# Optimization experiments

Hardware: AMD Instinct MI355X
Metric: run time of the kernel (lower is better)

The kernel has to match this reference:

```python
import jax, jax.numpy as jnp
import numpy as np

APERTURE = 256
IGNORE_ITSELF = False
FMAX = jnp.float32(3.4028235e38)  # tf.float32.max


def setup_inputs() -> dict:
    key = jax.random.key(0)
    ks = jax.random.split(key, 5)
    n, m, d = 4096, 1024, 1024
    scale = 1.0 / np.sqrt(m)
    x = jax.random.normal(ks[0], (n, m), dtype=jnp.float32)
    WK = jax.random.normal(ks[1], (m, d), dtype=jnp.float32) * scale
    WQ = jax.random.normal(ks[2], (m, d), dtype=jnp.float32) * scale
    WV = jax.random.normal(ks[3], (m, d), dtype=jnp.float32) * scale
    Wout = jax.random.normal(ks[4], (d, m), dtype=jnp.float32) * scale
    return {"x": x, "WK": WK, "WQ": WQ, "WV": WV, "Wout": Wout}


def reference(x, WK, WQ, WV, Wout):
    n = x.shape[0]
    K = x @ WK                      # [n, d]
    Q = (x @ WQ) * 0.06             # [n, d]
    V = x @ WV                      # [n, d]
    logits = Q @ K.T                # [n, n]

    i = jnp.arange(n)[:, None]
    j = jnp.arange(n)[None, :]
    if IGNORE_ITSELF:
        keep = (i != j).astype(jnp.float32)
        logits = logits * keep - FMAX * (1.0 - keep)
    if APERTURE > 0:
        # tf: mask = 1 - band_part(ones, -aperture, aperture); negative num_lower
        # keeps the whole lower triangle, so mask==1 exactly where j - i > aperture.
        keep = (j - i > APERTURE).astype(jnp.float32)
        logits = logits * keep - FMAX * (1.0 - keep)

    att_weights = jax.nn.softmax(logits, axis=-1)  # [n, n]
    # dropout is identity (training=False). NOTE faithful quirk: transpose_a=True.
    y = att_weights.T @ V           # [n, d]
    y = y @ Wout                    # [n, m]
    return (y, att_weights)
```

## Files before the change

kernel.cpp:

```cpp
#include <hip/hip_runtime.h>
#include <cstdint>
#include <cstddef>

#define N_TOK 4096
#define M_DIM 1024
#define APER  256
#define UNIF_START 3839

typedef __attribute__((ext_vector_type(8))) short short8;
typedef __attribute__((ext_vector_type(4))) float float4_t;

__device__ __forceinline__ unsigned short f2bf(float x) {
    union { float f; uint32_t u; } v; v.f = x;
    uint32_t u = v.u;
    u += 0x7FFFu + ((u >> 16) & 1u);
    return (unsigned short)(u >> 16);
}

__device__ __forceinline__ void gload16(const void* g, void* l) {
    __builtin_amdgcn_global_load_lds(
        (const __attribute__((address_space(1))) void*)g,
        (__attribute__((address_space(3))) void*)l, 16, 0, 0);
}

__global__ __launch_bounds__(256) void cast_bf16(const float* __restrict__ src,
                                                 unsigned short* __restrict__ dst, int n) {
    const int i = (blockIdx.x * 256 + threadIdx.x) * 4;
    if (i >= n) return;
    const float4 v = *reinterpret_cast<const float4*>(&src[i]);
    ushort4 o;
    o.x = f2bf(v.x); o.y = f2bf(v.y); o.z = f2bf(v.z); o.w = f2bf(v.w);
    *reinterpret_cast<ushort4*>(&dst[i]) = o;
}

__global__ __launch_bounds__(256) void wtrans3(const float* __restrict__ W0, const float* __restrict__ W1,
                                               const float* __restrict__ W2,
                                               unsigned short* __restrict__ D0, unsigned short* __restrict__ D1,
                                               unsigned short* __restrict__ D2) {
    const int z = blockIdx.z;
    const float* src = z == 0 ? W0 : (z == 1 ? W1 : W2);
    unsigned short* dst = z == 0 ? D0 : (z == 1 ? D1 : D2);
    __shared__ unsigned short tile[32][33];
    const int c0 = blockIdx.x * 32, r0 = blockIdx.y * 32;
    const int tx = threadIdx.x & 31, ty = threadIdx.x >> 5;
#pragma unroll
    for (int i = ty; i < 32; i += 8)
        tile[i][tx] = f2bf(src[(size_t)(r0 + i) * M_DIM + c0 + tx]);
    __syncthreads();
#pragma unroll
    for (int i = ty; i < 32; i += 8)
        dst[(size_t)(c0 + i) * M_DIM + r0 + tx] = tile[tx][i];
}

__global__ __launch_bounds__(256) void transpose_bf16(const unsigned short* __restrict__ src,
                                                      unsigned short* __restrict__ dst,
                                                      int R, int C) {
    __shared__ unsigned short tile[32][33];
    const int c0 = blockIdx.x * 32, r0 = blockIdx.y * 32;
    const int tx = threadIdx.x & 31, ty = threadIdx.x >> 5;
#pragma unroll
    for (int i = ty; i < 32; i += 8)
        tile[i][tx] = src[(size_t)(r0 + i) * C + c0 + tx];
    __syncthreads();
#pragma unroll
    for (int i = ty; i < 32; i += 8)
        dst[(size_t)(c0 + i) * R + r0 + tx] = tile[tx][i];
}

template <int SKIP>
__global__ __launch_bounds__(256) void nt64sq(const unsigned short* __restrict__ A,
                                              const unsigned short* __restrict__ B,
                                              float* __restrict__ Cf,
                                              unsigned short* __restrict__ Cb,
                                              int N, int K) {
    const int by   = (SKIP == 1) ? ((int)gridDim.y - 1 - (int)blockIdx.y) : (int)blockIdx.y;
    const int row0 = by * 64;
    const int col0 = blockIdx.x * 64;

    __shared__ unsigned short Asb[64 * 32];
    __shared__ unsigned short Bsb[64 * 32];

    const int t = threadIdx.x, w = t >> 6, lane = t & 63;
    float4_t acc[4] = {};

    const int sr   = lane >> 2;
    const int sk   = ((lane & 3) ^ ((sr >> 1) & 3)) * 8;
    const int m    = lane & 15;
    const int slot = ((lane >> 4) ^ ((m >> 1) & 3)) * 8;

    for (int k0 = 0; k0 < K; k0 += 32) {
        if (SKIP == 1) {
            if ((k0 > row0 + 63 - APER - 1) && (k0 + 31 < UNIF_START)) continue;
        }
        const int rr = w * 16 + sr;
        gload16(&A[(size_t)(row0 + rr) * K + k0 + sk], &Asb[w * 512]);
        gload16(&B[(size_t)(col0 + rr) * K + k0 + sk], &Bsb[w * 512]);
        __syncthreads();
        const short8 af = *reinterpret_cast<const short8*>(&Asb[(w * 16 + m) * 32 + slot]);
        short8 bf[4];
#pragma unroll
        for (int j = 0; j < 4; ++j)
            bf[j] = *reinterpret_cast<const short8*>(&Bsb[(j * 16 + m) * 32 + slot]);
#pragma unroll
        for (int j = 0; j < 4; ++j)
            acc[j] = __builtin_amdgcn_mfma_f32_16x16x32_bf16(af, bf[j], acc[j], 0, 0, 0);
        __syncthreads();
    }

    const int crow = row0 + w * 16 + (lane >> 4) * 4;
    const int ccol = col0 + m;
#pragma unroll
    for (int j = 0; j < 4; ++j)
#pragma unroll
        for (int r = 0; r < 4; ++r) {
            const float v = acc[j][r];
            const size_t idx = (size_t)(crow + r) * N + ccol + j * 16;
            if (Cf) Cf[idx] = v;
            if (Cb) Cb[idx] = f2bf(v);
        }
}

__global__ __launch_bounds__(256) void atv_db(const unsigned short* __restrict__ A,
                                              const unsigned short* __restrict__ B,
                                              float* __restrict__ C) {
    const int by   = (int)gridDim.y - 1 - (int)blockIdx.y;
    const int row0 = by * 64;
    const int col0 = blockIdx.x * 128;

    __shared__ unsigned short As[2][64 * 64];
    __shared__ unsigned short Bs[2][128 * 64];

    const int t = threadIdx.x, w = t >> 6, lane = t & 63;
    const int wr = (w >> 1) * 32, wc = (w & 1) * 64;
    const int q = lane >> 4, m = lane & 15;

    const int srow = lane >> 3;
    const int schk = ((lane & 7) ^ (srow & 7)) * 8;

    int aoff[2][2], boff[4][2];
#pragma unroll
    for (int i = 0; i < 2; ++i)
#pragma unroll
        for (int h = 0; h < 2; ++h)
            aoff[i][h] = (wr + i * 16 + m) * 64 + (((h * 4 + q) ^ (m & 7)) * 8);
#pragma unroll
    for (int j = 0; j < 4; ++j)
#pragma unroll
        for (int h = 0; h < 2; ++h)
            boff[j][h] = (wc + j * 16 + m) * 64 + (((h * 4 + q) ^ (m & 7)) * 8);

    const int limit = row0 - 194;
    int nPre = (limit >= 0) ? (limit / 64 + 1) : 0;
    if (nPre > 59) nPre = 59;
    const int nT = nPre + 5;

    float4_t acc[2][4] = {};

    auto kof = [&](int s) { return s < nPre ? s * 64 : 3776 + (s - nPre) * 64; };

    auto stage = [&](int buf, int k0) {
#pragma unroll
        for (int c = 0; c < 2; ++c) {
            const int r0 = w * 16 + c * 8;
            gload16(&A[(size_t)(row0 + r0 + srow) * (size_t)N_TOK + k0 + schk],
                    &As[buf][r0 * 64]);
        }
#pragma unroll
        for (int c = 0; c < 4; ++c) {
            const int r0 = w * 32 + c * 8;
            gload16(&B[(size_t)(col0 + r0 + srow) * (size_t)N_TOK + k0 + schk],
                    &Bs[buf][r0 * 64]);
        }
    };

    stage(0, kof(0));
    __syncthreads();

    int cur = 0;
    for (int s = 0; s < nT; ++s) {
        if (s + 1 < nT) stage(cur ^ 1, kof(s + 1));
        short8 af[2][2], bf[4][2];
#pragma unroll
        for (int i = 0; i < 2; ++i)
#pragma unroll
            for (int h = 0; h < 2; ++h)
                af[i][h] = *reinterpret_cast<const short8*>(&As[cur][aoff[i][h]]);
#pragma unroll
        for (int j = 0; j < 4; ++j)
#pragma unroll
            for (int h = 0; h < 2; ++h)
                bf[j][h] = *reinterpret_cast<const short8*>(&Bs[cur][boff[j][h]]);
#pragma unroll
        for (int i = 0; i < 2; ++i)
#pragma unroll
            for (int j = 0; j < 4; ++j)
#pragma unroll
                for (int h = 0; h < 2; ++h)
                    acc[i][j] = __builtin_amdgcn_mfma_f32_16x16x32_bf16(af[i][h], bf[j][h],
                                                                        acc[i][j], 0, 0, 0);
        __syncthreads();
        cur ^= 1;
    }

#pragma unroll
    for (int i = 0; i < 2; ++i)
#pragma unroll
        for (int j = 0; j < 4; ++j)
#pragma unroll
            for (int r = 0; r < 4; ++r)
                C[(size_t)(row0 + wr + i * 16 + q * 4 + r) * M_DIM + col0 + wc + j * 16 + m] =
                    acc[i][j][r];
}

__global__ __launch_bounds__(256) void logits_db(const unsigned short* __restrict__ A,
                                                 const unsigned short* __restrict__ B,
                                                 float* __restrict__ att,
                                                 float* __restrict__ rowsum) {
    const int row0 = blockIdx.y * 64;
    const int col0 = blockIdx.x * 128;
    if (col0 + 127 <= row0 + APER) return;

    __shared__ unsigned short As[2][64 * 64];
    __shared__ unsigned short Bs[2][128 * 64];

    const int t = threadIdx.x, w = t >> 6, lane = t & 63;
    const int wr = (w >> 1) * 32, wc = (w & 1) * 64;
    const int q = lane >> 4, m = lane & 15;

    const int srow = lane >> 3;
    const int schk = ((lane & 7) ^ (srow & 7)) * 8;

    int aoff[2][2], boff[4][2];
#pragma unroll
    for (int i = 0; i < 2; ++i)
#pragma unroll
        for (int h = 0; h < 2; ++h)
            aoff[i][h] = (wr + i * 16 + m) * 64 + (((h * 4 + q) ^ (m & 7)) * 8);
#pragma unroll
    for (int j = 0; j < 4; ++j)
#pragma unroll
        for (int h = 0; h < 2; ++h)
            boff[j][h] = (wc + j * 16 + m) * 64 + (((h * 4 + q) ^ (m & 7)) * 8);

    float4_t acc[2][4] = {};

    auto stage = [&](int buf, int k0) {
#pragma unroll
        for (int c = 0; c < 2; ++c) {
            const int r0 = w * 16 + c * 8;
            gload16(&A[(size_t)(row0 + r0 + srow) * M_DIM + k0 + schk], &As[buf][r0 * 64]);
        }
#pragma unroll
        for (int c = 0; c < 4; ++c) {
            const int r0 = w * 32 + c * 8;
            gload16(&B[(size_t)(col0 + r0 + srow) * M_DIM + k0 + schk], &Bs[buf][r0 * 64]);
        }
    };

    stage(0, 0);
    __syncthreads();

    int cur = 0;
    for (int s = 0; s < 16; ++s) {
        if (s + 1 < 16) stage(cur ^ 1, (s + 1) * 64);
        short8 af[2][2], bf[4][2];
#pragma unroll
        for (int i = 0; i < 2; ++i)
#pragma unroll
            for (int h = 0; h < 2; ++h)
                af[i][h] = *reinterpret_cast<const short8*>(&As[cur][aoff[i][h]]);
#pragma unroll
        for (int j = 0; j < 4; ++j)
#pragma unroll
            for (int h = 0; h < 2; ++h)
                bf[j][h] = *reinterpret_cast<const short8*>(&Bs[cur][boff[j][h]]);
#pragma unroll
        for (int i = 0; i < 2; ++i)
#pragma unroll
            for (int j = 0; j < 4; ++j)
#pragma unroll
                for (int h = 0; h < 2; ++h)
                    acc[i][j] = __builtin_amdgcn_mfma_f32_16x16x32_bf16(af[i][h], bf[j][h],
                                                                        acc[i][j], 0, 0, 0);
        __syncthreads();
        cur ^= 1;
    }

#pragma unroll
    for (int i = 0; i < 2; ++i) {
#pragma unroll
        for (int r = 0; r < 4; ++r) {
            const int gr = row0 + wr + i * 16 + q * 4 + r;
            float partial = 0.0f;
#pragma unroll
            for (int j = 0; j < 4; ++j) {
                const int gc = col0 + wc + j * 16 + m;
                float val;
                if (gr >= UNIF_START) {
                    val = 1.0f;
                } else if (gc > gr + APER) {
                    val = __expf(acc[i][j][r]);
                    partial += val;
                } else {
                    val = 0.0f;
                }
                att[(size_t)gr * N_TOK + gc] = val;
            }
            partial += __shfl_xor(partial, 1, 64);
            partial += __shfl_xor(partial, 2, 64);
            partial += __shfl_xor(partial, 4, 64);
            partial += __shfl_xor(partial, 8, 64);
            if (m == 0 && gr < UNIF_START) atomicAdd(&rowsum[gr], partial);
        }
    }
}

__global__ __launch_bounds__(256) void mfma_qkv(const unsigned short* __restrict__ xb,
                                                const unsigned short* __restrict__ WKt,
                                                const unsigned short* __restrict__ WQt,
                                                const unsigned short* __restrict__ WVWt,
                                                unsigned short* __restrict__ Kb,
                                                unsigned short* __restrict__ Qb,
                                                unsigned short* __restrict__ VWb) {
    const int row0  = blockIdx.y * 128;
    const int col0g = blockIdx.x * 128;
    const int seg   = col0g >> 10;
    const int col0  = col0g & 1023;
    const unsigned short* B = seg == 0 ? WKt : (seg == 1 ? WQt : WVWt);
    unsigned short*       C = seg == 0 ? Kb  : (seg == 1 ? Qb  : VWb);
    const float alpha = (seg == 1) ? 0.06f : 1.0f;

    __shared__ unsigned short Asb[128 * 32];
    __shared__ unsigned short Bsb[128 * 32];

    const int t = threadIdx.x, w = t >> 6, lane = t & 63;
    const int wr = (w >> 1) * 64, wc = (w & 1) * 64;

    float4_t acc[4][4] = {};

    const int sr   = lane >> 2;
    const int sk   = ((lane & 3) ^ ((sr >> 1) & 3)) * 8;
    const int m    = lane & 15;
    const int slot = ((lane >> 4) ^ ((m >> 1) & 3)) * 8;

    for (int k0 = 0; k0 < M_DIM; k0 += 32) {
#pragma unroll
        for (int cc = 0; cc < 2; ++cc) {
            const int c = 2 * w + cc;
            const int rr = c * 16 + sr;
            gload16(&xb[(size_t)(row0 + rr) * M_DIM + k0 + sk], &Asb[c * 512]);
            gload16(&B[(size_t)(col0 + rr) * M_DIM + k0 + sk], &Bsb[c * 512]);
        }
        __syncthreads();
        short8 af[4], bf[4];
#pragma unroll
        for (int i = 0; i < 4; ++i)
            af[i] = *reinterpret_cast<const short8*>(&Asb[(wr + i * 16 + m) * 32 + slot]);
#pragma unroll
        for (int j = 0; j < 4; ++j)
            bf[j] = *reinterpret_cast<const short8*>(&Bsb[(wc + j * 16 + m) * 32 + slot]);
#pragma unroll
        for (int i = 0; i < 4; ++i)
#pragma unroll
            for (int j = 0; j < 4; ++j)
                acc[i][j] = __builtin_amdgcn_mfma_f32_16x16x32_bf16(af[i], bf[j], acc[i][j], 0, 0, 0);
        __syncthreads();
    }

    const int crow = row0 + wr + (lane >> 4) * 4;
    const int ccol = col0 + wc + m;
#pragma unroll
    for (int i = 0; i < 4; ++i)
#pragma unroll
        for (int j = 0; j < 4; ++j)
#pragma unroll
            for (int r = 0; r < 4; ++r)
                C[(size_t)(crow + i * 16 + r) * M_DIM + ccol + j * 16] = f2bf(alpha * acc[i][j][r]);
}

__global__ __launch_bounds__(256) void init_rowsum(float* __restrict__ rowsum) {
    const int i = blockIdx.x * 256 + threadIdx.x;
    if (i < N_TOK) rowsum[i] = (i >= UNIF_START) ? (float)N_TOK : 0.0f;
}

__global__ __launch_bounds__(256) void finalize_att(float* __restrict__ att,
                                                    unsigned short* __restrict__ attT,
                                                    const float* __restrict__ rowsum) {
    const int j0 = blockIdx.x * 64, i0 = blockIdx.y * 64;
    const int t = threadIdx.x;
    const int rl = t >> 4;
    const int c4 = (t & 15) * 4;
    const float u = 1.0f / (float)N_TOK;

    if (j0 + 63 <= i0 + APER) {
#pragma unroll
        for (int s = 0; s < 4; ++s) {
            const int i = i0 + rl + 16 * s;
            const float val = (i >= UNIF_START) ? u : 0.0f;
            float4 v; v.x = v.y = v.z = v.w = val;
            *reinterpret_cast<float4*>(&att[(size_t)i * N_TOK + j0 + c4]) = v;
        }
        const unsigned short bu = f2bf(u);
#pragma unroll
        for (int s = 0; s < 4; ++s) {
            const int j = j0 + rl + 16 * s;
            ushort4 o;
            o.x = (i0 + c4 + 0 >= UNIF_START) ? bu : 0;
            o.y = (i0 + c4 + 1 >= UNIF_START) ? bu : 0;
            o.z = (i0 + c4 + 2 >= UNIF_START) ? bu : 0;
            o.w = (i0 + c4 + 3 >= UNIF_START) ? bu : 0;
            *reinterpret_cast<ushort4*>(&attT[(size_t)j * N_TOK + i0 + c4]) = o;
        }
        return;
    }

    __shared__ unsigned short tile[64][72];
#pragma unroll
    for (int s = 0; s < 4; ++s) {
        const int il = rl + 16 * s;
        const int i  = i0 + il;
        const float inv = 1.0f / rowsum[i];
        float4 v = *reinterpret_cast<const float4*>(&att[(size_t)i * N_TOK + j0 + c4]);
        v.x *= inv; v.y *= inv; v.z *= inv; v.w *= inv;
        *reinterpret_cast<float4*>(&att[(size_t)i * N_TOK + j0 + c4]) = v;
        ushort4 b;
        b.x = f2bf(v.x); b.y = f2bf(v.y); b.z = f2bf(v.z); b.w = f2bf(v.w);
        *reinterpret_cast<ushort4*>(&tile[il][c4]) = b;
    }
    __syncthreads();
#pragma unroll
    for (int s = 0; s < 4; ++s) {
        const int jl = rl + 16 * s;
        ushort4 o;
        o.x = tile[c4 + 0][jl];
        o.y = tile[c4 + 1][jl];
        o.z = tile[c4 + 2][jl];
        o.w = tile[c4 + 3][jl];
        *reinterpret_cast<ushort4*>(&attT[(size_t)(j0 + jl) * N_TOK + i0 + c4]) = o;
    }
}

extern "C" void kernel_launch(void* const* d_in, const int* in_sizes, int n_in,
                              void* d_out, int out_size, void* d_ws, size_t ws_size,
                              hipStream_t stream) {
    const float* x    = (const float*)d_in[0];
    const float* WK   = (const float*)d_in[1];
    const float* WQ   = (const float*)d_in[2];
    const float* WV   = (const float*)d_in[3];
    const float* Wout = (const float*)d_in[4];

    float* y   = (float*)d_out;
    float* att = y + (size_t)N_TOK * M_DIM;

    unsigned short* base = (unsigned short*)d_ws;
    const size_t MEG = 1u << 20;
    unsigned short* xb    = base;
    unsigned short* WKt   = base + 4  * MEG;
    unsigned short* WQt   = base + 5  * MEG;
    unsigned short* Woutt = base + 6  * MEG;
    unsigned short* WVb   = base + 7  * MEG;
    unsigned short* WVWt  = base + 8  * MEG;
    unsigned short* Kb    = base + 9  * MEG;
    unsigned short* Qb    = base + 13 * MEG;
    unsigned short* VWb   = base + 17 * MEG;
    unsigned short* attT  = base + 4  * MEG;
    float*          rowsum = (float*)(base + 20 * MEG);
    unsigned short* VWt   = xb;

    const dim3 blk(256);

    cast_bf16<<<dim3((N_TOK * M_DIM) / 1024), blk, 0, stream>>>(x, xb, N_TOK * M_DIM);
    cast_bf16<<<dim3((M_DIM * M_DIM) / 1024), blk, 0, stream>>>(WV, WVb, M_DIM * M_DIM);
    wtrans3<<<dim3(M_DIM / 32, M_DIM / 32, 3), blk, 0, stream>>>(WK, WQ, Wout, WKt, WQt, Woutt);

    nt64sq<0><<<dim3(M_DIM / 64, M_DIM / 64), blk, 0, stream>>>(Woutt, WVb, nullptr, WVWt,
                                                                M_DIM, M_DIM);

    mfma_qkv<<<dim3(24, N_TOK / 128), blk, 0, stream>>>(xb, WKt, WQt, WVWt, Kb, Qb, VWb);

    transpose_bf16<<<dim3(M_DIM / 32, N_TOK / 32), blk, 0, stream>>>(VWb, VWt, N_TOK, M_DIM);

    init_rowsum<<<dim3(N_TOK / 256), blk, 0, stream>>>(rowsum);
    logits_db<<<dim3(N_TOK / 128, N_TOK / 64), blk, 0, stream>>>(Qb, Kb, att, rowsum);

    finalize_att<<<dim3(N_TOK / 64, N_TOK / 64), blk, 0, stream>>>(att, attT, rowsum);

    atv_db<<<dim3(M_DIM / 128, N_TOK / 64), blk, 0, stream>>>(attT, VWt, y);
}
```

Before: 298.1 us.

## Triple-buffer LDS staging in logits and atv GEMMs with partial vmcnt waits

Moves the logits and att^T·V GEMM kernels from double-buffered to triple-buffered LDS staging. Loads are issued two k-tiles ahead, and each iteration waits only until the oldest tile's six async global-to-LDS loads have landed (vmcnt(6)) before a raw barrier. The goal is to keep more memory traffic in flight and hide global load latency behind MFMA work. In exchange, LDS use per block rises by half, which may lower occupancy, and correctness now depends on the hand-written vmcnt counts matching the number of loads issued.

```diff
diff --git a/kernel.cpp b/kernel.cpp
--- a/kernel.cpp
+++ b/kernel.cpp
@@ -127,8 +127,8 @@
     const int row0 = by * 64;
     const int col0 = blockIdx.x * 128;
 
-    __shared__ unsigned short As[2][64 * 64];
-    __shared__ unsigned short Bs[2][128 * 64];
+    __shared__ unsigned short As[3][64 * 64];
+    __shared__ unsigned short Bs[3][128 * 64];
 
     const int t = threadIdx.x, w = t >> 6, lane = t & 63;
     const int wr = (w >> 1) * 32, wc = (w & 1) * 64;
@@ -174,22 +174,24 @@
     };
 
     stage(0, kof(0));
-    __syncthreads();
-
-    int cur = 0;
+    stage(1, kof(1));
+    asm volatile("s_waitcnt vmcnt(6)" ::: "memory");
+    __builtin_amdgcn_s_barrier();
+
     for (int s = 0; s < nT; ++s) {
-        if (s + 1 < nT) stage(cur ^ 1, kof(s + 1));
+        const int cb = s % 3;
+        if (s + 2 < nT) stage((s + 2) % 3, kof(s + 2));
         short8 af[2][2], bf[4][2];
 #pragma unroll
         for (int i = 0; i < 2; ++i)
 #pragma unroll
             for (int h = 0; h < 2; ++h)
-                af[i][h] = *reinterpret_cast<const short8*>(&As[cur][aoff[i][h]]);
+                af[i][h] = *reinterpret_cast<const short8*>(&As[cb][aoff[i][h]]);
 #pragma unroll
         for (int j = 0; j < 4; ++j)
 #pragma unroll
             for (int h = 0; h < 2; ++h)
-                bf[j][h] = *reinterpret_cast<const short8*>(&Bs[cur][boff[j][h]]);
+                bf[j][h] = *reinterpret_cast<const short8*>(&Bs[cb][boff[j][h]]);
 #pragma unroll
         for (int i = 0; i < 2; ++i)
 #pragma unroll
@@ -198,8 +200,11 @@
                 for (int h = 0; h < 2; ++h)
                     acc[i][j] = __builtin_amdgcn_mfma_f32_16x16x32_bf16(af[i][h], bf[j][h],
                                                                         acc[i][j], 0, 0, 0);
-        __syncthreads();
-        cur ^= 1;
+        if (s + 1 < nT) {
+            if (s + 2 < nT) asm volatile("s_waitcnt vmcnt(6)" ::: "memory");
+            else            asm volatile("s_waitcnt vmcnt(0)" ::: "memory");
+            __builtin_amdgcn_s_barrier();
+        }
     }
 
 #pragma unroll
@@ -220,8 +225,8 @@
     const int col0 = blockIdx.x * 128;
     if (col0 + 127 <= row0 + APER) return;
 
-    __shared__ unsigned short As[2][64 * 64];
-    __shared__ unsigned short Bs[2][128 * 64];
+    __shared__ unsigned short As[3][64 * 64];
+    __shared__ unsigned short Bs[3][128 * 64];
 
     const int t = threadIdx.x, w = t >> 6, lane = t & 63;
     const int wr = (w >> 1) * 32, wc = (w & 1) * 64;
@@ -258,22 +263,24 @@
     };
 
     stage(0, 0);
-    __syncthreads();
-
-    int cur = 0;
+    stage(1, 64);
+    asm volatile("s_waitcnt vmcnt(6)" ::: "memory");
+    __builtin_amdgcn_s_barrier();
+
     for (int s = 0; s < 16; ++s) {
-        if (s + 1 < 16) stage(cur ^ 1, (s + 1) * 64);
+        const int cb = s % 3;
+        if (s + 2 < 16) stage((s + 2) % 3, (s + 2) * 64);
         short8 af[2][2], bf[4][2];
 #pragma unroll
         for (int i = 0; i < 2; ++i)
 #pragma unroll
             for (int h = 0; h < 2; ++h)
-                af[i][h] = *reinterpret_cast<const short8*>(&As[cur][aoff[i][h]]);
+                af[i][h] = *reinterpret_cast<const short8*>(&As[cb][aoff[i][h]]);
 #pragma unroll
         for (int j = 0; j < 4; ++j)
 #pragma unroll
             for (int h = 0; h < 2; ++h)
-                bf[j][h] = *reinterpret_cast<const short8*>(&Bs[cur][boff[j][h]]);
+                bf[j][h] = *reinterpret_cast<const short8*>(&Bs[cb][boff[j][h]]);
 #pragma unroll
         for (int i = 0; i < 2; ++i)
 #pragma unroll
@@ -282,8 +289,11 @@
                 for (int h = 0; h < 2; ++h)
                     acc[i][j] = __builtin_amdgcn_mfma_f32_16x16x32_bf16(af[i][h], bf[j][h],
                                                                         acc[i][j], 0, 0, 0);
-        __syncthreads();
-        cur ^= 1;
+        if (s + 1 < 16) {
+            if (s + 2 < 16) asm volatile("s_waitcnt vmcnt(6)" ::: "memory");
+            else            asm volatile("s_waitcnt vmcnt(0)" ::: "memory");
+            __builtin_amdgcn_s_barrier();
+        }
     }
 
 #pragma unroll
```

Result: slower. 305.2 us (+2.4%).
